# Performance work log

Measured on AMD Instinct MI355X. Metric: run time of the kernel, lower is better.

Reference implementation:

```python
import jax, jax.numpy as jnp
import numpy as np
import math

NUM_HEADS = 12


def _rope_tables(nph, npw, half_head_dim):
    # grid coords: x = column index, y = row index, flattened row-major
    rows = jnp.arange(nph, dtype=jnp.float32)
    cols = jnp.arange(npw, dtype=jnp.float32)
    gy, gx = jnp.meshgrid(rows, cols, indexing='ij')
    coords = jnp.stack([gx.ravel(), gy.ravel()], axis=1)  # [N, 2]
    cmin = coords.min(axis=0, keepdims=True)
    cmax = coords.max(axis=0, keepdims=True)
    nc = (coords - cmin) / (cmax - cmin + 1e-8)
    div = jnp.exp(jnp.arange(0, half_head_dim, 2, dtype=jnp.float32)
                  * (-(math.log(10000.0) / half_head_dim)))  # [half/2]
    px = nc[:, 0:1] * div  # [N, half/2]
    py = nc[:, 1:2] * div
    rep = lambda t: jnp.repeat(t, 2, axis=-1)  # interleave: even/odd slots get same value
    return rep(jnp.cos(px)), rep(jnp.sin(px)), rep(jnp.cos(py)), rep(jnp.sin(py))


def _apply_rope(t, cos_x, sin_x, cos_y, sin_y):
    # t: [B, H, N, Dh]; tables: [N, Dh//2] broadcast over B, H
    half = t.shape[-1] // 2
    tx, ty = t[..., :half], t[..., half:]
    rx = tx * cos_x + jnp.roll(tx, 1, axis=-1) * sin_x
    ry = ty * cos_y + jnp.roll(ty, 1, axis=-1) * sin_y
    return jnp.concatenate([rx, ry], axis=-1)


def setup_inputs() -> dict:
    key = jax.random.key(0)
    k1, k2, k3 = jax.random.split(key, 3)
    B, S, E = 32, 577, 768  # 24*24 patches + 1 CLS token
    x = jax.random.normal(k1, (B, S, E), dtype=jnp.float32)
    w_qkv = jax.random.normal(k2, (3 * E, E), dtype=jnp.float32) * 0.02
    w_proj = jax.random.normal(k3, (E, E), dtype=jnp.float32) * 0.02
    return {"x": x, "w_qkv": w_qkv, "w_proj": w_proj,
            "num_patches_h": 24, "num_patches_w": 24}


def reference(x, w_qkv, w_proj, num_patches_h, num_patches_w):
    B, S, E = x.shape
    H = NUM_HEADS
    Dh = E // H
    # QKV projection (bias=False)
    qkv = jnp.einsum('bse,fe->bsf', x, w_qkv).reshape(B, S, 3, H, Dh)
    qkv = jnp.transpose(qkv, (2, 0, 3, 1, 4))  # [3, B, H, S, Dh]
    q, k, v = qkv[0], qkv[1], qkv[2]
    # 2D RoPE on patch tokens only (CLS at position 0 unchanged)
    cx, sx, cy, sy = _rope_tables(num_patches_h, num_patches_w, Dh // 2)
    q_patch = _apply_rope(q[:, :, 1:], cx, sx, cy, sy)
    k_patch = _apply_rope(k[:, :, 1:], cx, sx, cy, sy)
    q = jnp.concatenate([q[:, :, :1], q_patch], axis=2)
    k = jnp.concatenate([k[:, :, :1], k_patch], axis=2)
    # scaled dot-product attention (standard backend, dropout=0)
    attn = jnp.einsum('bhqd,bhkd->bhqk', q, k) * (Dh ** -0.5)
    attn = jax.nn.softmax(attn, axis=-1)
    out = jnp.einsum('bhqk,bhkd->bhqd', attn, v)
    out = jnp.transpose(out, (0, 2, 1, 3)).reshape(B, S, E)
    return out @ w_proj.T
```

## Files before the change

kernel.cpp:

```cpp
#include <hip/hip_runtime.h>
#include <hip/hip_bf16.h>
#include <cstdint>


typedef __attribute__((ext_vector_type(8))) short bf16x8;
typedef __attribute__((ext_vector_type(4))) float f32x4;

#define MFMA16(a, b, c) __builtin_amdgcn_mfma_f32_16x16x32_bf16((a), (b), (c), 0, 0, 0)

#define S_LEN 577
#define NHEAD 12
#define DHEAD 64
#define EMB   768
#define F3    2304
#define NT_KV 10
#define BUFO  (128 * 32)

__device__ __forceinline__ void gload_lds16(const __hip_bfloat16* g, __hip_bfloat16* l) {
    __builtin_amdgcn_global_load_lds(
        (const __attribute__((address_space(1))) unsigned int*)g,
        (__attribute__((address_space(3))) unsigned int*)l, 16, 0, 0);
}

__device__ __forceinline__ uint4 cvt8_f32(float4 a, float4 b) {
    union { uint4 u; __hip_bfloat16 h[8]; } r;
    r.h[0] = __float2bfloat16(a.x); r.h[1] = __float2bfloat16(a.y);
    r.h[2] = __float2bfloat16(a.z); r.h[3] = __float2bfloat16(a.w);
    r.h[4] = __float2bfloat16(b.x); r.h[5] = __float2bfloat16(b.y);
    r.h[6] = __float2bfloat16(b.z); r.h[7] = __float2bfloat16(b.w);
    return r.u;
}

__device__ __forceinline__ uint4 load8_f32(const float* p) {
    return cvt8_f32(*(const float4*)p, *(const float4*)(p + 4));
}

__global__ __launch_bounds__(256) void cvt_f32_bf16(
    const float* __restrict__ src, __hip_bfloat16* __restrict__ dst, int n8)
{
    const int i = blockIdx.x * 256 + threadIdx.x;
    if (i < n8)
        *(uint4*)(dst + (size_t)i * 8) = load8_f32(src + (size_t)i * 8);
}

template<bool AF32, bool BF32, bool CF32>
__global__ __launch_bounds__(256) void gemm_a_dma(
    const void* __restrict__ Av, int lda,
    const void* __restrict__ Bv, int ldb,
    void* __restrict__ Cv, int M, int N, int K)
{
    __shared__ __hip_bfloat16 As[2 * BUFO];
    __shared__ __hip_bfloat16 Bs[2 * BUFO];

    const int t      = threadIdx.x;
    const int l      = t & 63;
    const int w      = t >> 6;
    const int lane15 = l & 15;
    const int quad   = l >> 4;

    const int n0 = blockIdx.x * 128;
    const int m0 = blockIdx.y * 128;
    const int wm = (w >> 1) * 64;
    const int wn = (w & 1) * 64;

    const int srow   = t >> 2;
    const int schunk = t & 3;
    const int fsw    = (t >> 3) & 3;
    const int gchunk = schunk ^ fsw;

    int ar0 = m0 + srow;       if (ar0 > M - 1) ar0 = M - 1;
    int ar1 = m0 + 64 + srow;  if (ar1 > M - 1) ar1 = M - 1;
    const int br0 = n0 + srow;
    const int br1 = n0 + 64 + srow;

    const size_t a0off = (size_t)ar0 * lda + gchunk * 8;
    const size_t a1off = (size_t)ar1 * lda + gchunk * 8;
    const size_t b0off = (size_t)br0 * ldb + gchunk * 8;
    const size_t b1off = (size_t)br1 * ldb + gchunk * 8;

    __hip_bfloat16* lAs0 = As + srow * 32 + schunk * 8;
    __hip_bfloat16* lAs1 = As + (64 + srow) * 32 + schunk * 8;
    __hip_bfloat16* lBs0 = Bs + srow * 32 + schunk * 8;
    __hip_bfloat16* lBs1 = Bs + (64 + srow) * 32 + schunk * 8;

    const int rsw = (quad ^ ((lane15 >> 1) & 3)) * 8;

    f32x4 acc[4][4] = {};

    if constexpr (AF32) {
        const float* qa0 = (const float*)Av + a0off;
        const float* qa1 = (const float*)Av + a1off;
        *(uint4*)lAs0 = cvt8_f32(*(const float4*)qa0, *(const float4*)(qa0 + 4));
        *(uint4*)lAs1 = cvt8_f32(*(const float4*)qa1, *(const float4*)(qa1 + 4));
    } else {
        gload_lds16((const __hip_bfloat16*)Av + a0off, lAs0);
        gload_lds16((const __hip_bfloat16*)Av + a1off, lAs1);
    }
    if constexpr (BF32) {
        const float* pb0 = (const float*)Bv + b0off;
        const float* pb1 = (const float*)Bv + b1off;
        *(uint4*)lBs0 = cvt8_f32(*(const float4*)pb0, *(const float4*)(pb0 + 4));
        *(uint4*)lBs1 = cvt8_f32(*(const float4*)pb1, *(const float4*)(pb1 + 4));
    } else {
        gload_lds16((const __hip_bfloat16*)Bv + b0off, lBs0);
        gload_lds16((const __hip_bfloat16*)Bv + b1off, lBs1);
    }
    __syncthreads();

#define GEMM_STEP(kn, CO, NO)                                                 \
    {                                                                         \
        const bool has_next = (kn) < K;                                       \
        float4 a0 = {}, a1 = {}, a2 = {}, a3 = {};                            \
        float4 g0 = {}, g1 = {}, g2 = {}, g3 = {};                            \
        if (has_next) {                                                       \
            if constexpr (AF32) {                                             \
                const float* qa0 = (const float*)Av + a0off + (kn);           \
                const float* qa1 = (const float*)Av + a1off + (kn);           \
                a0 = *(const float4*)qa0; a1 = *(const float4*)(qa0 + 4);     \
                a2 = *(const float4*)qa1; a3 = *(const float4*)(qa1 + 4);     \
            } else {                                                          \
                gload_lds16((const __hip_bfloat16*)Av + a0off + (kn), lAs0 + (NO)); \
                gload_lds16((const __hip_bfloat16*)Av + a1off + (kn), lAs1 + (NO)); \
            }                                                                 \
            if constexpr (BF32) {                                             \
                const float* pb0 = (const float*)Bv + b0off + (kn);           \
                const float* pb1 = (const float*)Bv + b1off + (kn);           \
                g0 = *(const float4*)pb0; g1 = *(const float4*)(pb0 + 4);     \
                g2 = *(const float4*)pb1; g3 = *(const float4*)(pb1 + 4);     \
            } else {                                                          \
                gload_lds16((const __hip_bfloat16*)Bv + b0off + (kn), lBs0 + (NO)); \
                gload_lds16((const __hip_bfloat16*)Bv + b1off + (kn), lBs1 + (NO)); \
            }                                                                 \
        }                                                                     \
        bf16x8 a[4], b[4];                                                    \
        _Pragma("unroll")                                                     \
        for (int i = 0; i < 4; ++i)                                           \
            a[i] = *(const bf16x8*)(As + (CO) + (wm + i * 16 + lane15) * 32 + rsw); \
        _Pragma("unroll")                                                     \
        for (int j = 0; j < 4; ++j)                                           \
            b[j] = *(const bf16x8*)(Bs + (CO) + (wn + j * 16 + lane15) * 32 + rsw); \
        _Pragma("unroll")                                                     \
        for (int i = 0; i < 4; ++i)                                           \
            _Pragma("unroll")                                                 \
            for (int j = 0; j < 4; ++j)                                       \
                acc[i][j] = MFMA16(a[i], b[j], acc[i][j]);                    \
        if (has_next) {                                                       \
            if constexpr (AF32) {                                             \
                *(uint4*)(lAs0 + (NO)) = cvt8_f32(a0, a1);                    \
                *(uint4*)(lAs1 + (NO)) = cvt8_f32(a2, a3);                    \
            }                                                                 \
            if constexpr (BF32) {                                             \
                *(uint4*)(lBs0 + (NO)) = cvt8_f32(g0, g1);                    \
                *(uint4*)(lBs1 + (NO)) = cvt8_f32(g2, g3);                    \
            }                                                                 \
        }                                                                     \
        __syncthreads();                                                      \
    }

    for (int k0 = 0; k0 < K; k0 += 64) {
        GEMM_STEP(k0 + 32, 0,    BUFO)
        GEMM_STEP(k0 + 64, BUFO, 0)
    }
#undef GEMM_STEP

    #pragma unroll
    for (int i = 0; i < 4; ++i) {
        #pragma unroll
        for (int r = 0; r < 4; ++r) {
            const int m = m0 + wm + i * 16 + quad * 4 + r;
            if (m < M) {
                #pragma unroll
                for (int j = 0; j < 4; ++j) {
                    const int n = n0 + wn + j * 16 + lane15;
                    if constexpr (CF32)
                        ((float*)Cv)[(size_t)m * N + n] = acc[i][j][r];
                    else
                        ((__hip_bfloat16*)Cv)[(size_t)m * N + n] = __float2bfloat16(acc[i][j][r]);
                }
            }
        }
    }
}

__global__ __launch_bounds__(256) void rope_kernel(__hip_bfloat16* __restrict__ qkv)
{
    const int p = blockIdx.x;
    const int b = blockIdx.y;
    const int l = threadIdx.x & 63;
    const int w = threadIdx.x >> 6;

    const int jj   = l & 31;
    const float i2 = (float)((jj >> 1) * 2);
    const float dv = __expf(-i2 * 0.28782313662425576f);
    const float inv = 1.0f / (23.0f + 1e-8f);
    const float cx = (float)(p % 24) * inv;
    const float cy = (float)(p / 24) * inv;
    const float ang = ((l < 32) ? cx : cy) * dv;
    const float c = __cosf(ang);
    const float s = __sinf(ang);
    const int nb = (l & 32) | ((jj + 31) & 31);

    const size_t rowbase = ((size_t)(b * S_LEN + 1 + p)) * F3;

    for (int pr = w; pr < 24; pr += 4) {
        const int part = pr / 12;
        const int h    = pr % 12;
        const size_t off = rowbase + (size_t)part * EMB + h * DHEAD + l;
        float v  = __bfloat162float(qkv[off]);
        float vp = __shfl(v, nb, 64);
        qkv[off] = __float2bfloat16(v * c + vp * s);
    }
}

__global__ __launch_bounds__(512) void attn_kernel(
    const __hip_bfloat16* __restrict__ qkv,
    __hip_bfloat16* __restrict__ attn_out, int ldo)
{
    __shared__ __hip_bfloat16 Qs[128][72];
    __shared__ __hip_bfloat16 Ks[64][72];
    __shared__ __hip_bfloat16 Vt[64][72];

    const int t      = threadIdx.x;
    const int l      = t & 63;
    const int w      = t >> 6;
    const int lane15 = l & 15;
    const int quad   = l >> 4;

    const int q0 = blockIdx.x * 128;
    const int h  = blockIdx.y;
    const int b  = blockIdx.z;

    const int krow = t >> 3, kseg = t & 7;
    const int vs   = t & 63, vdg = t >> 6;

    uint4 ku, vu;
    {
        int gk = krow; if (gk > S_LEN - 1) gk = S_LEN - 1;
        ku = ((const uint4*)(qkv + (size_t)(b * S_LEN + gk) * F3 + EMB + h * DHEAD))[kseg];
        int gv = vs;  if (gv > S_LEN - 1) gv = S_LEN - 1;
        vu = ((const uint4*)(qkv + (size_t)(b * S_LEN + gv) * F3 + 2 * EMB + h * DHEAD))[vdg];
    }

    {
        const int row = t >> 2, seg = t & 3;
        int gq = q0 + row; if (gq > S_LEN - 1) gq = S_LEN - 1;
        const uint4* src = (const uint4*)(qkv + (size_t)(b * S_LEN + gq) * F3 + h * DHEAD + seg * 16);
        uint4 u0 = src[0], u1 = src[1];
        const __hip_bfloat16* e0 = (const __hip_bfloat16*)&u0;
        const __hip_bfloat16* e1 = (const __hip_bfloat16*)&u1;
        #pragma unroll
        for (int i = 0; i < 8; ++i) {
            Qs[row][seg * 16 + i]     = __float2bfloat16(__bfloat162float(e0[i]) * 0.125f);
            Qs[row][seg * 16 + 8 + i] = __float2bfloat16(__bfloat162float(e1[i]) * 0.125f);
        }
    }
    __syncthreads();

    bf16x8 qf0 = *(const bf16x8*)&Qs[w * 16 + lane15][quad * 8];
    bf16x8 qf1 = *(const bf16x8*)&Qs[w * 16 + lane15][32 + quad * 8];

    f32x4 o[4] = {};
    float m_i = -3.0e38f;
    float l_i = 0.f;

    for (int ti = 0; ti < NT_KV; ++ti) {
        __syncthreads();
        *(uint4*)&Ks[krow][kseg * 8] = ku;
        {
            const __hip_bfloat16* e0 = (const __hip_bfloat16*)&vu;
            #pragma unroll
            for (int i = 0; i < 8; ++i)
                Vt[vdg * 8 + i][vs] = e0[i];
        }
        if (ti + 1 < NT_KV) {
            int gk = (ti + 1) * 64 + krow; if (gk > S_LEN - 1) gk = S_LEN - 1;
            ku = ((const uint4*)(qkv + (size_t)(b * S_LEN + gk) * F3 + EMB + h * DHEAD))[kseg];
            int gv = (ti + 1) * 64 + vs;  if (gv > S_LEN - 1) gv = S_LEN - 1;
            vu = ((const uint4*)(qkv + (size_t)(b * S_LEN + gv) * F3 + 2 * EMB + h * DHEAD))[vdg];
        }
        asm volatile("s_waitcnt lgkmcnt(0)" ::: "memory");
        __builtin_amdgcn_s_barrier();
        asm volatile("" ::: "memory");

        f32x4 sf[4];
        __builtin_amdgcn_s_setprio(1);
        #pragma unroll
        for (int nt = 0; nt < 4; ++nt) {
            f32x4 z = {0.f, 0.f, 0.f, 0.f};
            bf16x8 k0f = *(const bf16x8*)&Ks[nt * 16 + lane15][quad * 8];
            bf16x8 k1f = *(const bf16x8*)&Ks[nt * 16 + lane15][32 + quad * 8];
            z = MFMA16(k0f, qf0, z);
            z = MFMA16(k1f, qf1, z);
            sf[nt] = z;
        }
        __builtin_amdgcn_s_setprio(0);
        const int s0 = ti * 64;
        #pragma unroll
        for (int nt = 0; nt < 4; ++nt)
            #pragma unroll
            for (int r = 0; r < 4; ++r)
                if (s0 + nt * 16 + quad * 4 + r >= S_LEN) sf[nt][r] = -1e30f;

        float mx = fmaxf(fmaxf(sf[0][0], sf[0][1]), fmaxf(sf[0][2], sf[0][3]));
        #pragma unroll
        for (int nt = 1; nt < 4; ++nt)
            mx = fmaxf(mx, fmaxf(fmaxf(sf[nt][0], sf[nt][1]), fmaxf(sf[nt][2], sf[nt][3])));
        mx = fmaxf(mx, __shfl_xor(mx, 16, 64));
        mx = fmaxf(mx, __shfl_xor(mx, 32, 64));

        if (!__all(mx - m_i <= 8.0f)) {
            const float mnew  = fmaxf(m_i, mx);
            const float alpha = __expf(m_i - mnew);
            m_i = mnew;
            l_i *= alpha;
            float af[4];
            #pragma unroll
            for (int r = 0; r < 4; ++r)
                af[r] = __shfl(alpha, quad * 4 + r, 64);
            #pragma unroll
            for (int ci = 0; ci < 4; ++ci)
                #pragma unroll
                for (int r = 0; r < 4; ++r)
                    o[ci][r] *= af[r];
        }

        float sum = 0.f;
        #pragma unroll
        for (int nt = 0; nt < 4; ++nt) {
            #pragma unroll
            for (int r = 0; r < 4; ++r) {
                sf[nt][r] = __expf(sf[nt][r] - m_i);
                sum += sf[nt][r];
            }
        }
        sum += __shfl_xor(sum, 16, 64);
        sum += __shfl_xor(sum, 32, 64);
        l_i += sum;

        #pragma unroll
        for (int nt = 0; nt < 4; ++nt)
            #pragma unroll
            for (int r = 0; r < 4; ++r)
                Qs[w * 16 + lane15][nt * 16 + quad * 4 + r] = __float2bfloat16(sf[nt][r]);
        asm volatile("s_waitcnt lgkmcnt(0)" ::: "memory");

        __builtin_amdgcn_s_setprio(1);
        #pragma unroll
        for (int s32 = 0; s32 < 2; ++s32) {
            bf16x8 pa = *(const bf16x8*)&Qs[w * 16 + lane15][s32 * 32 + quad * 8];
            #pragma unroll
            for (int ci = 0; ci < 4; ++ci) {
                bf16x8 vb = *(const bf16x8*)&Vt[ci * 16 + lane15][s32 * 32 + quad * 8];
                o[ci] = MFMA16(pa, vb, o[ci]);
            }
        }
        __builtin_amdgcn_s_setprio(0);
    }

    #pragma unroll
    for (int r = 0; r < 4; ++r) {
        const float lr = __shfl(l_i, quad * 4 + r, 64);
        const int q = q0 + w * 16 + quad * 4 + r;
        if (q < S_LEN) {
            const float rl = 1.0f / lr;
            #pragma unroll
            for (int ci = 0; ci < 4; ++ci) {
                attn_out[(size_t)(b * S_LEN + q) * ldo + h * DHEAD + ci * 16 + lane15] =
                    __float2bfloat16(o[ci][r] * rl);
            }
        }
    }
}

extern "C" void kernel_launch(void* const* d_in, const int* in_sizes, int n_in,
                              void* d_out, int out_size, void* d_ws, size_t ws_size,
                              hipStream_t stream) {
    const float* x      = (const float*)d_in[0];
    const float* w_qkv  = (const float*)d_in[1];
    const float* w_proj = (const float*)d_in[2];
    for (int i = 0; i < n_in; ++i) {
        if      (in_sizes[i] == 32 * S_LEN * EMB) x      = (const float*)d_in[i];
        else if (in_sizes[i] == F3 * EMB)         w_qkv  = (const float*)d_in[i];
        else if (in_sizes[i] == EMB * EMB)        w_proj = (const float*)d_in[i];
    }
    float* out = (float*)d_out;

    const int Mrows = 32 * S_LEN;
    const int NX    = Mrows * EMB;
    const int NWQ   = F3 * EMB;

    __hip_bfloat16* qkv = (__hip_bfloat16*)d_ws;
    __hip_bfloat16* xb  = (__hip_bfloat16*)d_out;
    __hip_bfloat16* wb  = xb + (size_t)NX;

    cvt_f32_bf16<<<NX / 8 / 256, 256, 0, stream>>>(x, xb, NX / 8);
    cvt_f32_bf16<<<NWQ / 8 / 256, 256, 0, stream>>>(w_qkv, wb, NWQ / 8);
    gemm_a_dma<false, false, false><<<dim3(F3 / 128, (Mrows + 127) / 128), 256, 0, stream>>>(
        xb, EMB, wb, EMB, qkv, Mrows, F3, EMB);
    rope_kernel<<<dim3(576, 32), 256, 0, stream>>>(qkv);
    attn_kernel<<<dim3((S_LEN + 127) / 128, NHEAD, 32), 512, 0, stream>>>(qkv, qkv, F3);
    gemm_a_dma<false, true, true><<<dim3(EMB / 128, (Mrows + 127) / 128), 256, 0, stream>>>(
        qkv, F3, w_proj, EMB, out, Mrows, EMB, EMB);
}
```

Measured before the change: 388.0 us.

## Fuse RoPE into attention Q/K staging and merge conversion kernels

Removes the standalone RoPE kernel, which read and wrote Q and K in global memory, and applies the rotation inline when Q is staged into shared memory and when each K tile is written to shared memory. Neighbour elements needed for the roll are taken with lane shuffles. The two fp32-to-bf16 conversion launches are also merged into one grid. The cost is that K rotation (including sin/cos) is now recomputed for every query block and head that reads it, adding ALU work inside the attention loop.

Measured after the change: 366.6 us. 5.5% less time.

```diff
diff --git a/kernel.cpp b/kernel.cpp
--- a/kernel.cpp
+++ b/kernel.cpp
@@ -15,6 +15,7 @@
 #define F3    2304
 #define NT_KV 10
 #define BUFO  (128 * 32)
+#define LN1E4_32 0.28782313662425576f
 
 __device__ __forceinline__ void gload_lds16(const __hip_bfloat16* g, __hip_bfloat16* l) {
     __builtin_amdgcn_global_load_lds(
@@ -35,12 +36,20 @@
     return cvt8_f32(*(const float4*)p, *(const float4*)(p + 4));
 }
 
-__global__ __launch_bounds__(256) void cvt_f32_bf16(
-    const float* __restrict__ src, __hip_bfloat16* __restrict__ dst, int n8)
+__global__ __launch_bounds__(256) void cvt_pair(
+    const float* __restrict__ xs, __hip_bfloat16* __restrict__ xd, int nx8,
+    const float* __restrict__ ws, __hip_bfloat16* __restrict__ wd, int nw8,
+    int xblocks)
 {
-    const int i = blockIdx.x * 256 + threadIdx.x;
-    if (i < n8)
-        *(uint4*)(dst + (size_t)i * 8) = load8_f32(src + (size_t)i * 8);
+    if ((int)blockIdx.x < xblocks) {
+        const int i = blockIdx.x * 256 + threadIdx.x;
+        if (i < nx8)
+            *(uint4*)(xd + (size_t)i * 8) = load8_f32(xs + (size_t)i * 8);
+    } else {
+        const int i = (blockIdx.x - xblocks) * 256 + threadIdx.x;
+        if (i < nw8)
+            *(uint4*)(wd + (size_t)i * 8) = load8_f32(ws + (size_t)i * 8);
+    }
 }
 
 template<bool AF32, bool BF32, bool CF32>
@@ -182,36 +191,6 @@
     }
 }
 
-__global__ __launch_bounds__(256) void rope_kernel(__hip_bfloat16* __restrict__ qkv)
-{
-    const int p = blockIdx.x;
-    const int b = blockIdx.y;
-    const int l = threadIdx.x & 63;
-    const int w = threadIdx.x >> 6;
-
-    const int jj   = l & 31;
-    const float i2 = (float)((jj >> 1) * 2);
-    const float dv = __expf(-i2 * 0.28782313662425576f);
-    const float inv = 1.0f / (23.0f + 1e-8f);
-    const float cx = (float)(p % 24) * inv;
-    const float cy = (float)(p / 24) * inv;
-    const float ang = ((l < 32) ? cx : cy) * dv;
-    const float c = __cosf(ang);
-    const float s = __sinf(ang);
-    const int nb = (l & 32) | ((jj + 31) & 31);
-
-    const size_t rowbase = ((size_t)(b * S_LEN + 1 + p)) * F3;
-
-    for (int pr = w; pr < 24; pr += 4) {
-        const int part = pr / 12;
-        const int h    = pr % 12;
-        const size_t off = rowbase + (size_t)part * EMB + h * DHEAD + l;
-        float v  = __bfloat162float(qkv[off]);
-        float vp = __shfl(v, nb, 64);
-        qkv[off] = __float2bfloat16(v * c + vp * s);
-    }
-}
-
 __global__ __launch_bounds__(512) void attn_kernel(
     const __hip_bfloat16* __restrict__ qkv,
     __hip_bfloat16* __restrict__ attn_out, int ldo)
@@ -233,6 +212,13 @@
     const int krow = t >> 3, kseg = t & 7;
     const int vs   = t & 63, vdg = t >> 6;
 
+    const float cinv = 1.0f / (23.0f + 1e-8f);
+    float dvk[4];
+    #pragma unroll
+    for (int m = 0; m < 4; ++m)
+        dvk[m] = __expf(-(float)(2 * ((kseg & 3) * 4 + m)) * LN1E4_32);
+    const int ksrc = ((kseg & 3) == 0) ? (l + 3) : (l - 1);
+
     uint4 ku, vu;
     {
         int gk = krow; if (gk > S_LEN - 1) gk = S_LEN - 1;
@@ -244,15 +230,29 @@
     {
         const int row = t >> 2, seg = t & 3;
         int gq = q0 + row; if (gq > S_LEN - 1) gq = S_LEN - 1;
-        const uint4* src = (const uint4*)(qkv + (size_t)(b * S_LEN + gq) * F3 + h * DHEAD + seg * 16);
-        uint4 u0 = src[0], u1 = src[1];
-        const __hip_bfloat16* e0 = (const __hip_bfloat16*)&u0;
-        const __hip_bfloat16* e1 = (const __hip_bfloat16*)&u1;
-        #pragma unroll
-        for (int i = 0; i < 8; ++i) {
-            Qs[row][seg * 16 + i]     = __float2bfloat16(__bfloat162float(e0[i]) * 0.125f);
-            Qs[row][seg * 16 + 8 + i] = __float2bfloat16(__bfloat162float(e1[i]) * 0.125f);
-        }
+        const uint4* src4 = (const uint4*)(qkv + (size_t)(b * S_LEN + gq) * F3 + h * DHEAD + seg * 16);
+        union { uint4 u[2]; __hip_bfloat16 hh[16]; } qi;
+        qi.u[0] = src4[0]; qi.u[1] = src4[1];
+        float v[16];
+        #pragma unroll
+        for (int i = 0; i < 16; ++i) v[i] = __bfloat162float(qi.hh[i]);
+        const float ext = __shfl(v[15], l ^ 1, 64);
+        const bool no_rope = (gq == 0);
+        const int p = no_rope ? 0 : gq - 1;
+        const float coord = ((seg >= 2) ? (float)(p / 24) : (float)(p % 24)) * cinv;
+        union { uint4 u[2]; __hip_bfloat16 hh[16]; } qo;
+        #pragma unroll
+        for (int m = 0; m < 8; ++m) {
+            const float dv = __expf(-(float)(2 * ((seg & 1) * 8 + m)) * LN1E4_32);
+            const float ang = coord * dv;
+            const float c1 = no_rope ? 1.0f : __cosf(ang);
+            const float s1 = no_rope ? 0.0f : __sinf(ang);
+            const float pe = (m == 0) ? ext : v[2 * m - 1];
+            qo.hh[2 * m]     = __float2bfloat16((v[2 * m]     * c1 + pe       * s1) * 0.125f);
+            qo.hh[2 * m + 1] = __float2bfloat16((v[2 * m + 1] * c1 + v[2 * m] * s1) * 0.125f);
+        }
+        *(uint4*)&Qs[row][seg * 16]     = qo.u[0];
+        *(uint4*)&Qs[row][seg * 16 + 8] = qo.u[1];
     }
     __syncthreads();
 
@@ -265,7 +265,29 @@
 
     for (int ti = 0; ti < NT_KV; ++ti) {
         __syncthreads();
-        *(uint4*)&Ks[krow][kseg * 8] = ku;
+        {
+            int gk = ti * 64 + krow; if (gk > S_LEN - 1) gk = S_LEN - 1;
+            union { uint4 u; __hip_bfloat16 hh[8]; } ki;
+            ki.u = ku;
+            float v[8];
+            #pragma unroll
+            for (int i = 0; i < 8; ++i) v[i] = __bfloat162float(ki.hh[i]);
+            const float ext = __shfl(v[7], ksrc, 64);
+            const bool no_rope = (gk == 0);
+            const int p = no_rope ? 0 : gk - 1;
+            const float coord = ((kseg >= 4) ? (float)(p / 24) : (float)(p % 24)) * cinv;
+            union { uint4 u; __hip_bfloat16 hh[8]; } ko;
+            #pragma unroll
+            for (int m = 0; m < 4; ++m) {
+                const float ang = coord * dvk[m];
+                const float c1 = no_rope ? 1.0f : __cosf(ang);
+                const float s1 = no_rope ? 0.0f : __sinf(ang);
+                const float pe = (m == 0) ? ext : v[2 * m - 1];
+                ko.hh[2 * m]     = __float2bfloat16(v[2 * m]     * c1 + pe       * s1);
+                ko.hh[2 * m + 1] = __float2bfloat16(v[2 * m + 1] * c1 + v[2 * m] * s1);
+            }
+            *(uint4*)&Ks[krow][kseg * 8] = ko.u;
+        }
         {
             const __hip_bfloat16* e0 = (const __hip_bfloat16*)&vu;
             #pragma unroll
@@ -393,11 +415,11 @@
     __hip_bfloat16* xb  = (__hip_bfloat16*)d_out;
     __hip_bfloat16* wb  = xb + (size_t)NX;
 
-    cvt_f32_bf16<<<NX / 8 / 256, 256, 0, stream>>>(x, xb, NX / 8);
-    cvt_f32_bf16<<<NWQ / 8 / 256, 256, 0, stream>>>(w_qkv, wb, NWQ / 8);
+    const int xblocks = NX / 8 / 256;
+    const int wblocks = NWQ / 8 / 256;
+    cvt_pair<<<xblocks + wblocks, 256, 0, stream>>>(x, xb, NX / 8, w_qkv, wb, NWQ / 8, xblocks);
     gemm_a_dma<false, false, false><<<dim3(F3 / 128, (Mrows + 127) / 128), 256, 0, stream>>>(
         xb, EMB, wb, EMB, qkv, Mrows, F3, EMB);
-    rope_kernel<<<dim3(576, 32), 256, 0, stream>>>(qkv);
     attn_kernel<<<dim3((S_LEN + 127) / 128, NHEAD, 32), 512, 0, stream>>>(qkv, qkv, F3);
     gemm_a_dma<false, true, true><<<dim3(EMB / 128, (Mrows + 127) / 128), 256, 0, stream>>>(
         qkv, F3, w_proj, EMB, out, Mrows, EMB, EMB);
```
